# Performance work log

Hardware: AMD Instinct MI355X
Metric: run time of the kernel (lower is better)

The kernel has to match this reference:

```python
import jax, jax.numpy as jnp
import numpy as np

D_MODEL = 2048
N_HEADS = 16
D_HEAD = D_MODEL // N_HEADS
D_FF = 8192
EPS = 1e-5


def _xavier(key, shape):
    fan_out, fan_in = shape
    limit = np.sqrt(6.0 / (fan_in + fan_out))
    return jax.random.uniform(key, shape, jnp.float32, -limit, limit)


def setup_inputs() -> dict:
    key = jax.random.key(0)
    ks = jax.random.split(key, 6)
    B, S = 2, 2048
    x = jax.random.normal(ks[0], (B, S, D_MODEL), jnp.float32)
    # additive causal mask: 0 on/below diagonal, -inf above
    causal = jnp.tril(jnp.ones((S, S), jnp.bool_))
    mask = jnp.where(causal, 0.0, -1e9).astype(jnp.float32)
    return {
        "x": x,
        "mask": mask,
        "Wqkv": _xavier(ks[1], (3 * D_MODEL, D_MODEL)),
        "Wo": _xavier(ks[2], (D_MODEL, D_MODEL)),
        "w1": _xavier(ks[3], (D_FF, D_MODEL)),
        "w2": _xavier(ks[4], (D_MODEL, D_FF)),
        "ln1_g": jnp.ones((D_MODEL,), jnp.float32),
        "ln1_b": jnp.zeros((D_MODEL,), jnp.float32),
        "ln2_g": jnp.ones((D_MODEL,), jnp.float32),
        "ln2_b": jnp.zeros((D_MODEL,), jnp.float32),
    }


def _layernorm(x, g, b):
    mu = jnp.mean(x, axis=-1, keepdims=True)
    var = jnp.mean(jnp.square(x - mu), axis=-1, keepdims=True)
    return (x - mu) * jax.lax.rsqrt(var + EPS) * g + b


def reference(x, mask, Wqkv, Wo, w1, w2, ln1_g, ln1_b, ln2_g, ln2_b):
    B, S, D = x.shape
    # --- attention sublayer (pre-norm) ---
    h = _layernorm(x, ln1_g, ln1_b)
    qkv = (h @ Wqkv.T).reshape(B, S, 3, N_HEADS, D_HEAD)
    q, k, v = qkv[:, :, 0], qkv[:, :, 1], qkv[:, :, 2]  # [B,S,H,Dh]
    scores = jnp.einsum("bqhd,bkhd->bhqk", q, k) / np.sqrt(D_HEAD)
    scores = scores + mask  # broadcast [S,S] over [B,H,S,S]
    attn = jax.nn.softmax(scores, axis=-1)
    out = jnp.einsum("bhqk,bkhd->bqhd", attn, v).reshape(B, S, D)
    x = x + out @ Wo.T
    # --- FFN sublayer (pre-norm) ---
    h = _layernorm(x, ln2_g, ln2_b)
    x = x + jax.nn.gelu(h @ w1.T, approximate=False) @ w2.T
    return x
```

## Files before the change

kernel.cpp:

```cpp
#include <hip/hip_runtime.h>
#include <hip/hip_bf16.h>
#include <cmath>

#define D_MODEL 2048
#define N_HEADS 16
#define D_HEAD 128
#define D_FF 8192
#define S_LEN 2048
#define BATCH 2

typedef short bf16x8 __attribute__((ext_vector_type(8)));
typedef float f32x4 __attribute__((ext_vector_type(4)));
typedef unsigned short ushort_t;

__device__ __forceinline__ ushort_t f2bf(float f) {
  __hip_bfloat16 b = __float2bfloat16(f);
  union { __hip_bfloat16 b; ushort_t u; } cvt;
  cvt.b = b;
  return cvt.u;
}

__device__ __forceinline__ void gload16(const void* g, void* l) {
  __builtin_amdgcn_global_load_lds(
      (const __attribute__((address_space(1))) unsigned int*)g,
      (__attribute__((address_space(3))) unsigned int*)l, 16, 0, 0);
}

__device__ __forceinline__ float gelu_f(float v) {
  return 0.5f * v * (1.0f + erff(v * 0.70710678118654752f));
}

__global__ __launch_bounds__(256) void ln_bf16_kernel(
    const float* __restrict__ x, const float* __restrict__ g,
    const float* __restrict__ bb, ushort_t* __restrict__ outB) {
  const int row = blockIdx.x;
  const int tid = threadIdx.x;
  const float4* xr = (const float4*)(x + (size_t)row * D_MODEL);
  float4 v0 = xr[tid];
  float4 v1 = xr[tid + 256];
  float s  = v0.x + v0.y + v0.z + v0.w + v1.x + v1.y + v1.z + v1.w;
  float ss = v0.x*v0.x + v0.y*v0.y + v0.z*v0.z + v0.w*v0.w
           + v1.x*v1.x + v1.y*v1.y + v1.z*v1.z + v1.w*v1.w;
#pragma unroll
  for (int off = 32; off > 0; off >>= 1) {
    s  += __shfl_down(s, off);
    ss += __shfl_down(ss, off);
  }
  __shared__ float red[8];
  const int wid = tid >> 6;
  if ((tid & 63) == 0) { red[wid] = s; red[4 + wid] = ss; }
  __syncthreads();
  s  = red[0] + red[1] + red[2] + red[3];
  ss = red[4] + red[5] + red[6] + red[7];
  const float mu   = s * (1.0f / D_MODEL);
  const float var  = ss * (1.0f / D_MODEL) - mu * mu;
  const float rstd = rsqrtf(var + 1e-5f);
  const float4* gr = (const float4*)g;
  const float4* br = (const float4*)bb;
  float4 g0 = gr[tid], g1 = gr[tid + 256];
  float4 b0 = br[tid], b1 = br[tid + 256];
  ushort4 h0, h1;
  h0.x = f2bf((v0.x - mu) * rstd * g0.x + b0.x);
  h0.y = f2bf((v0.y - mu) * rstd * g0.y + b0.y);
  h0.z = f2bf((v0.z - mu) * rstd * g0.z + b0.z);
  h0.w = f2bf((v0.w - mu) * rstd * g0.w + b0.w);
  h1.x = f2bf((v1.x - mu) * rstd * g1.x + b1.x);
  h1.y = f2bf((v1.y - mu) * rstd * g1.y + b1.y);
  h1.z = f2bf((v1.z - mu) * rstd * g1.z + b1.z);
  h1.w = f2bf((v1.w - mu) * rstd * g1.w + b1.w);
  ushort4* oh = (ushort4*)(outB + (size_t)row * D_MODEL);
  oh[tid] = h0; oh[tid + 256] = h1;
}

__global__ __launch_bounds__(256) void wconv_kernel(
    const float* __restrict__ W, ushort_t* __restrict__ H, int n4) {
  for (int i = blockIdx.x * 256 + threadIdx.x; i < n4; i += gridDim.x * 256) {
    float4 v = ((const float4*)W)[i];
    ushort4 h;
    h.x = f2bf(v.x); h.y = f2bf(v.y); h.z = f2bf(v.z); h.w = f2bf(v.w);
    ((ushort4*)H)[i] = h;
  }
}

__global__ __launch_bounds__(256) void wconv_chunk_kernel(
    const float* __restrict__ W, ushort_t* __restrict__ H, int rows,
    int chunkCols, int rowStride, int colOff) {
  const int c4n = chunkCols >> 2;
  const int n4 = rows * c4n;
  for (int i = blockIdx.x * 256 + threadIdx.x; i < n4; i += gridDim.x * 256) {
    const int r = i / c4n, c4 = i - r * c4n;
    float4 v = *(const float4*)&W[(size_t)r * rowStride + colOff + c4 * 4];
    ushort4 h;
    h.x = f2bf(v.x); h.y = f2bf(v.y); h.z = f2bf(v.z); h.w = f2bf(v.w);
    ((ushort4*)H)[i] = h;
  }
}

template <int EPI>
__global__ __launch_bounds__(256, 4) void gemmb(
    const ushort_t* __restrict__ A, const ushort_t* __restrict__ B,
    const float* __restrict__ R, float* __restrict__ C,
    ushort_t* __restrict__ Cb, ushort_t* __restrict__ Q3,
    ushort_t* __restrict__ K3, ushort_t* __restrict__ V3,
    int M, int N, int K) {
  __shared__ char lds[2][16384];

  const int gX = gridDim.x;
  const int nwg = gX * gridDim.y;
  const int bid0 = blockIdx.y * gX + blockIdx.x;
  const int cpx = nwg >> 3;
  const int bid = (bid0 & 7) * cpx + (bid0 >> 3);
  const int bn0 = (bid % gX) * 128;
  const int bm0 = (bid / gX) * 128;

  const int tid = threadIdx.x;
  const int lane = tid & 63;
  const int wv = tid >> 6;
  const int wr = wv >> 1, wc = wv & 1;

  const int scs = (((lane & 7) ^ (lane >> 3)) << 4);
  const ushort_t* src = (wv < 2) ? A : B;
  const int rb0 = (wv < 2) ? bm0 : bn0;
  char* myLds = &lds[wv >> 1][0] + (wv & 1) * 8192;
  const ushort_t* srcBase =
      src + (size_t)(rb0 + (wv & 1) * 64 + (lane >> 3)) * K + (scs >> 1);

  const int l15 = lane & 15;
  const int swz = (lane & 7) << 4;
  const int cb0 = (((lane >> 4) * 16)) ^ swz;
  const int cb1 = (64 + ((lane >> 4) * 16)) ^ swz;

  f32x4 acc[4][4];
#pragma unroll
  for (int i = 0; i < 4; ++i)
#pragma unroll
    for (int j = 0; j < 4; ++j) acc[i][j] = (f32x4)0.0f;

  const char* ldsA = &lds[0][0];
  const char* ldsB = &lds[1][0];

  for (int kt = 0; kt < K; kt += 64) {
    {
      const ushort_t* g = srcBase + kt;
#pragma unroll
      for (int ch = 0; ch < 8; ++ch)
        gload16(g + (size_t)ch * 8 * K, myLds + ch * 1024);
    }
    __syncthreads();
#pragma unroll
    for (int ks = 0; ks < 2; ++ks) {
      const int cb = ks ? cb1 : cb0;
      bf16x8 af[4], bf[4];
#pragma unroll
      for (int mf = 0; mf < 4; ++mf)
        af[mf] = *(const bf16x8*)(ldsA + (wr * 64 + mf * 16 + l15) * 128 + cb);
#pragma unroll
      for (int nf = 0; nf < 4; ++nf)
        bf[nf] = *(const bf16x8*)(ldsB + (wc * 64 + nf * 16 + l15) * 128 + cb);
#pragma unroll
      for (int mf = 0; mf < 4; ++mf)
#pragma unroll
        for (int nf = 0; nf < 4; ++nf)
          acc[mf][nf] = __builtin_amdgcn_mfma_f32_16x16x32_bf16(
              af[mf], bf[nf], acc[mf][nf], 0, 0, 0);
    }
    __syncthreads();
  }

  const int orow = bm0 + wr * 64 + (lane >> 4) * 4;
  const int ocol = bn0 + wc * 64 + l15;
#pragma unroll
  for (int mf = 0; mf < 4; ++mf)
#pragma unroll
    for (int nf = 0; nf < 4; ++nf) {
      const f32x4 v = acc[mf][nf];
#pragma unroll
      for (int reg = 0; reg < 4; ++reg) {
        const int gr = orow + mf * 16 + reg;
        const int gcol = ocol + nf * 16;
        float f = v[reg];
        if (EPI == 1) {
          const size_t idx = (size_t)gr * N + gcol;
          C[idx] = f + R[idx];
        } else if (EPI == 2) {
          Cb[(size_t)gr * N + gcol] = f2bf(gelu_f(f));
        } else if (EPI == 3) {
          const ushort_t vb = f2bf(f);
          if (gcol < D_MODEL) {
            Q3[(size_t)gr * D_MODEL + gcol] = vb;
          } else {
            const int cc = gcol - D_MODEL;
            const bool isK = cc < D_MODEL;
            const int cc2 = isK ? cc : cc - D_MODEL;
            const int hh = cc2 >> 7, dd = cc2 & 127;
            const int bb = gr >> 11, ss = gr & 2047;
            const int tt = ss >> 6, rr = ss & 63;
            const size_t tb =
                ((size_t)((bb * N_HEADS + hh) * 32 + tt)) * 16384;
            if (isK) {
              const int byt = (rr * 256 + dd * 2) ^ ((rr & 7) << 4);
              *(ushort_t*)((char*)K3 + tb + byt) = vb;
            } else {
              const int byt = (dd * 128 + rr * 2) ^ ((dd & 7) << 4);
              *(ushort_t*)((char*)V3 + tb + byt) = vb;
            }
          }
        }
      }
    }
}

__global__ __launch_bounds__(256, 2) void attn_mfma_kernel(
    const ushort_t* __restrict__ Qc, const ushort_t* __restrict__ Kp,
    const ushort_t* __restrict__ Vp, ushort_t* __restrict__ outB) {
  const int pa = blockIdx.x, h = blockIdx.y, b = blockIdx.z;
  __shared__ char ldsK[16384];
  __shared__ char ldsVt[16384];
  __shared__ char ldsP[4][2048];
  const int tid = threadIdx.x, lane = tid & 63, w = tid >> 6;
  const int l15 = lane & 15, hi = lane >> 4;
  const int swzA = (l15 & 7) << 4;
  const float scale = 0.08838834764831845f;
  const size_t tbase0 = ((size_t)(b * N_HEADS + h) * 32) * 16384;

  for (int ph = 0; ph < 2; ++ph) {
    const int qc = ph ? (31 - pa) : pa;
    bf16x8 qf[4];
    {
      const int qrow = qc * 64 + w * 16 + l15;
      const ushort_t* qp =
          Qc + (size_t)(b * S_LEN + qrow) * D_MODEL + h * D_HEAD + hi * 8;
#pragma unroll
      for (int dt = 0; dt < 4; ++dt) qf[dt] = *(const bf16x8*)(qp + dt * 32);
    }
    float mrow[4], lrow[4];
#pragma unroll
    for (int r = 0; r < 4; ++r) { mrow[r] = -INFINITY; lrow[r] = 0.0f; }
    f32x4 oa[8];
#pragma unroll
    for (int dt = 0; dt < 8; ++dt) oa[dt] = (f32x4)0.0f;

    const int nkv = qc + 1;
    const int wqmax = qc * 64 + w * 16 + 15;

    for (int t = 0; t < nkv; ++t) {
      const int kv0 = t * 64;
      {
        const char* ks = (const char*)Kp + tbase0 + (size_t)t * 16384;
        const char* vs = (const char*)Vp + tbase0 + (size_t)t * 16384;
#pragma unroll
        for (int c = 0; c < 4; ++c) {
          gload16(ks + c * 4096 + tid * 16, ldsK + c * 4096 + tid * 16);
          gload16(vs + c * 4096 + tid * 16, ldsVt + c * 4096 + tid * 16);
        }
      }
      __syncthreads();
      if (kv0 <= wqmax) {
        f32x4 sa[4];
#pragma unroll
        for (int nt = 0; nt < 4; ++nt) sa[nt] = (f32x4)0.0f;
#pragma unroll
        for (int nt = 0; nt < 4; ++nt) {
          const int ro = (nt * 16 + l15) * 256;
#pragma unroll
          for (int dt = 0; dt < 4; ++dt) {
            bf16x8 kf =
                *(const bf16x8*)(ldsK + ro + ((dt * 64 + hi * 16) ^ swzA));
            sa[nt] = __builtin_amdgcn_mfma_f32_16x16x32_bf16(qf[dt], kf,
                                                             sa[nt], 0, 0, 0);
          }
        }
#pragma unroll
        for (int nt = 0; nt < 4; ++nt) {
          const int kg = kv0 + nt * 16 + l15;
#pragma unroll
          for (int r = 0; r < 4; ++r) {
            const int qg = qc * 64 + w * 16 + hi * 4 + r;
            float s = sa[nt][r] * scale;
            if (kg > qg) s -= 1e9f;
            sa[nt][r] = s;
          }
        }
        float frow[4];
#pragma unroll
        for (int r = 0; r < 4; ++r) {
          float tm = fmaxf(fmaxf(sa[0][r], sa[1][r]),
                           fmaxf(sa[2][r], sa[3][r]));
          tm = fmaxf(tm, __shfl_xor(tm, 1));
          tm = fmaxf(tm, __shfl_xor(tm, 2));
          tm = fmaxf(tm, __shfl_xor(tm, 4));
          tm = fmaxf(tm, __shfl_xor(tm, 8));
          const float mo = mrow[r];
          const float mn = fmaxf(mo, tm);
          const float fc = __expf(mo - mn);
          float sum = 0.0f;
#pragma unroll
          for (int nt = 0; nt < 4; ++nt) {
            const float p = __expf(sa[nt][r] - mn);
            sa[nt][r] = p;
            sum += p;
          }
          sum += __shfl_xor(sum, 1);
          sum += __shfl_xor(sum, 2);
          sum += __shfl_xor(sum, 4);
          sum += __shfl_xor(sum, 8);
          lrow[r] = lrow[r] * fc + sum;
          mrow[r] = mn;
          frow[r] = fc;
        }
        char* pw = ldsP[w];
#pragma unroll
        for (int r = 0; r < 4; ++r) {
          const int q = hi * 4 + r;
          const int qs = (q & 7) << 4;
#pragma unroll
          for (int nt = 0; nt < 4; ++nt) {
            const int byt = (q * 128 + (nt * 16 + l15) * 2) ^ qs;
            *(ushort_t*)(pw + byt) = f2bf(sa[nt][r]);
          }
        }
#pragma unroll
        for (int dt = 0; dt < 8; ++dt)
#pragma unroll
          for (int r = 0; r < 4; ++r) oa[dt][r] *= frow[r];
        bf16x8 pf[2];
#pragma unroll
        for (int kt = 0; kt < 2; ++kt)
          pf[kt] = *(const bf16x8*)(pw + (l15 * 128 +
                                          ((kt * 64 + hi * 16) ^ swzA)));
#pragma unroll
        for (int dt = 0; dt < 8; ++dt) {
          const int ro = (dt * 16 + l15) * 128;
#pragma unroll
          for (int kt = 0; kt < 2; ++kt) {
            bf16x8 vf =
                *(const bf16x8*)(ldsVt + ro + ((kt * 64 + hi * 16) ^ swzA));
            oa[dt] = __builtin_amdgcn_mfma_f32_16x16x32_bf16(pf[kt], vf,
                                                             oa[dt], 0, 0, 0);
          }
        }
      }
      __syncthreads();
    }
#pragma unroll
    for (int r = 0; r < 4; ++r) {
      const float linv = 1.0f / lrow[r];
      const size_t row = (size_t)(b * S_LEN + qc * 64 + w * 16 + hi * 4 + r);
#pragma unroll
      for (int dt = 0; dt < 8; ++dt) {
        const int col = h * D_HEAD + dt * 16 + l15;
        outB[row * D_MODEL + col] = f2bf(oa[dt][r] * linv);
      }
    }
  }
}

extern "C" void kernel_launch(void* const* d_in, const int* in_sizes, int n_in,
                              void* d_out, int out_size, void* d_ws,
                              size_t ws_size, hipStream_t stream) {
  const float* x    = (const float*)d_in[0];
  const float* Wqkv = (const float*)d_in[2];
  const float* Wo   = (const float*)d_in[3];
  const float* w1   = (const float*)d_in[4];
  const float* w2   = (const float*)d_in[5];
  const float* ln1g = (const float*)d_in[6];
  const float* ln1b = (const float*)d_in[7];
  const float* ln2g = (const float*)d_in[8];
  const float* ln2b = (const float*)d_in[9];
  float* out = (float*)d_out;

  const int M = BATCH * S_LEN;

  const size_t NEED = 92274688;
  if (ws_size < NEED) return;

  char* base = (char*)d_ws;
  ushort_t* WB  = (ushort_t*)base;
  ushort_t* act = (ushort_t*)(base + 25165824);
  ushort_t* Qc  = (ushort_t*)(base + 41943040);
  ushort_t* Kp  = (ushort_t*)(base + 58720256);
  ushort_t* Vp  = (ushort_t*)(base + 75497472);
  ushort_t* ffB = (ushort_t*)(base + 41943040);

  ln_bf16_kernel<<<M, 256, 0, stream>>>(x, ln1g, ln1b, act);
  wconv_kernel<<<2048, 256, 0, stream>>>(Wqkv, WB, 12582912 / 4);
  gemmb<3><<<dim3(3 * D_MODEL / 128, M / 128), 256, 0, stream>>>(
      act, WB, nullptr, nullptr, nullptr, Qc, Kp, Vp, M, 3 * D_MODEL, D_MODEL);
  attn_mfma_kernel<<<dim3(16, N_HEADS, BATCH), 256, 0, stream>>>(
      Qc, Kp, Vp, act);
  wconv_kernel<<<2048, 256, 0, stream>>>(Wo, WB, 4194304 / 4);
  gemmb<1><<<dim3(D_MODEL / 128, M / 128), 256, 0, stream>>>(
      act, WB, x, out, nullptr, nullptr, nullptr, nullptr,
      M, D_MODEL, D_MODEL);
  ln_bf16_kernel<<<M, 256, 0, stream>>>(out, ln2g, ln2b, act);
  for (int c = 0; c < 2; ++c) {
    wconv_kernel<<<2048, 256, 0, stream>>>(
        w1 + (size_t)c * 4096 * D_MODEL, WB, 8388608 / 4);
    gemmb<2><<<dim3(4096 / 128, M / 128), 256, 0, stream>>>(
        act, WB, nullptr, nullptr, ffB, nullptr, nullptr, nullptr,
        M, 4096, D_MODEL);
    wconv_chunk_kernel<<<2048, 256, 0, stream>>>(
        w2, WB, D_MODEL, 4096, D_FF, c * 4096);
    gemmb<1><<<dim3(D_MODEL / 128, M / 128), 256, 0, stream>>>(
        ffB, WB, out, out, nullptr, nullptr, nullptr, nullptr,
        M, D_MODEL, 4096);
  }
}
```

Measured before the change: 824.4 us.

## Replace GEMM with 8-wave 256-row tiled double-buffered pipelined kernel

Replaces the 128x128, 4-wave, single-buffered bf16 GEMM with a 512-thread kernel using 256xBN tiles (BN 256 or 128) and double-buffered LDS. Global-to-LDS loads for the next K tile are split into four stages interleaved with MFMA phases, using explicit vmcnt waits and raised wave priority. The aim is to hide global load latency and raise arithmetic intensity per block. In exchange it uses more LDS and registers per block, lowers occupancy, and produces fewer blocks for the smaller GEMMs.

```diff
diff --git a/kernel.cpp b/kernel.cpp
--- a/kernel.cpp
+++ b/kernel.cpp
@@ -28,6 +28,19 @@
 
 __device__ __forceinline__ float gelu_f(float v) {
   return 0.5f * v * (1.0f + erff(v * 0.70710678118654752f));
+}
+
+__device__ __forceinline__ void wait_vm4() {
+  asm volatile("s_waitcnt vmcnt(4)" ::: "memory");
+  __builtin_amdgcn_sched_barrier(0);
+}
+__device__ __forceinline__ void wait_vm3() {
+  asm volatile("s_waitcnt vmcnt(3)" ::: "memory");
+  __builtin_amdgcn_sched_barrier(0);
+}
+__device__ __forceinline__ void wait_vm0() {
+  asm volatile("s_waitcnt vmcnt(0)" ::: "memory");
+  __builtin_amdgcn_sched_barrier(0);
 }
 
 __global__ __launch_bounds__(256) void ln_bf16_kernel(
@@ -96,83 +109,150 @@
   }
 }
 
-template <int EPI>
-__global__ __launch_bounds__(256, 4) void gemmb(
+template <int EPI, int BN>
+__global__ __launch_bounds__(512, 2) void gemm8(
     const ushort_t* __restrict__ A, const ushort_t* __restrict__ B,
     const float* __restrict__ R, float* __restrict__ C,
     ushort_t* __restrict__ Cb, ushort_t* __restrict__ Q3,
     ushort_t* __restrict__ K3, ushort_t* __restrict__ V3,
     int M, int N, int K) {
-  __shared__ char lds[2][16384];
+  constexpr int APLANE = 16384;
+  constexpr int BPLANE = BN * 64;
+  constexpr int BUFSZ = 2 * APLANE + 2 * BPLANE;
+  constexpr int NF = BN / 64;
+  constexpr int WN = BN / 4;
+  __shared__ char lds[2 * BUFSZ];
 
   const int gX = gridDim.x;
   const int nwg = gX * gridDim.y;
   const int bid0 = blockIdx.y * gX + blockIdx.x;
   const int cpx = nwg >> 3;
   const int bid = (bid0 & 7) * cpx + (bid0 >> 3);
-  const int bn0 = (bid % gX) * 128;
-  const int bm0 = (bid / gX) * 128;
+  const int bn0 = (bid % gX) * BN;
+  const int bm0 = (bid / gX) * 256;
 
   const int tid = threadIdx.x;
   const int lane = tid & 63;
-  const int wv = tid >> 6;
-  const int wr = wv >> 1, wc = wv & 1;
-
-  const int scs = (((lane & 7) ^ (lane >> 3)) << 4);
-  const ushort_t* src = (wv < 2) ? A : B;
-  const int rb0 = (wv < 2) ? bm0 : bn0;
-  char* myLds = &lds[wv >> 1][0] + (wv & 1) * 8192;
-  const ushort_t* srcBase =
-      src + (size_t)(rb0 + (wv & 1) * 64 + (lane >> 3)) * K + (scs >> 1);
-
-  const int l15 = lane & 15;
-  const int swz = (lane & 7) << 4;
-  const int cb0 = (((lane >> 4) * 16)) ^ swz;
-  const int cb1 = (64 + ((lane >> 4) * 16)) ^ swz;
-
-  f32x4 acc[4][4];
-#pragma unroll
-  for (int i = 0; i < 4; ++i)
-#pragma unroll
-    for (int j = 0; j < 4; ++j) acc[i][j] = (f32x4)0.0f;
-
-  const char* ldsA = &lds[0][0];
-  const char* ldsB = &lds[1][0];
-
-  for (int kt = 0; kt < K; kt += 64) {
-    {
-      const ushort_t* g = srcBase + kt;
-#pragma unroll
-      for (int ch = 0; ch < 8; ++ch)
-        gload16(g + (size_t)ch * 8 * K, myLds + ch * 1024);
-    }
-    __syncthreads();
-#pragma unroll
-    for (int ks = 0; ks < 2; ++ks) {
-      const int cb = ks ? cb1 : cb0;
-      bf16x8 af[4], bf[4];
-#pragma unroll
-      for (int mf = 0; mf < 4; ++mf)
-        af[mf] = *(const bf16x8*)(ldsA + (wr * 64 + mf * 16 + l15) * 128 + cb);
-#pragma unroll
-      for (int nf = 0; nf < 4; ++nf)
-        bf[nf] = *(const bf16x8*)(ldsB + (wc * 64 + nf * 16 + l15) * 128 + cb);
-#pragma unroll
-      for (int mf = 0; mf < 4; ++mf)
-#pragma unroll
-        for (int nf = 0; nf < 4; ++nf)
-          acc[mf][nf] = __builtin_amdgcn_mfma_f32_16x16x32_bf16(
-              af[mf], bf[nf], acc[mf][nf], 0, 0, 0);
-    }
-    __syncthreads();
-  }
-
-  const int orow = bm0 + wr * 64 + (lane >> 4) * 4;
-  const int ocol = bn0 + wc * 64 + l15;
-#pragma unroll
-  for (int mf = 0; mf < 4; ++mf)
-#pragma unroll
-    for (int nf = 0; nf < 4; ++nf) {
+  const int wid = tid >> 6;
+  const int wm = wid >> 2, wn = wid & 3;
+  const int l15 = lane & 15, hi = lane >> 4;
+
+  const ushort_t* aSrc = A + (size_t)(bm0 + (tid >> 2)) * K + (tid & 3) * 8;
+  const ushort_t* bSrc = B + (size_t)(bn0 + (tid >> 2)) * K + (tid & 3) * 8;
+  const int ldsW = wid * 1024;
+
+  const int aFrag = (wm * 128 + l15) * 64 + hi * 16;
+  const int bFrag = (wn * WN + l15) * 64 + hi * 16;
+
+  f32x4 acc[8][NF];
+#pragma unroll
+  for (int i = 0; i < 8; ++i)
+#pragma unroll
+    for (int j = 0; j < NF; ++j) acc[i][j] = (f32x4)0.0f;
+
+  const int NT = K >> 6;
+
+  auto STAGE = [&](int u, int j) {
+    char* buf = lds + (u & 1) * BUFSZ;
+    const int kt = u * 64;
+    if (j & 1) {
+      const int ks = (j == 3);
+      char* d = buf + ks * APLANE + ldsW;
+      const ushort_t* s = aSrc + kt + ks * 32;
+      gload16(s, d);
+      gload16(s + (size_t)128 * K, d + 8192);
+    } else {
+      const int ks = (j == 2);
+      char* d = buf + 2 * APLANE + ks * BPLANE + ldsW;
+      const ushort_t* s = bSrc + kt + ks * 32;
+      gload16(s, d);
+      if (BN == 256) gload16(s + (size_t)128 * K, d + 8192);
+    }
+  };
+  auto WAIT_STEADY = [&]() { if (BN == 256) wait_vm4(); else wait_vm3(); };
+
+  STAGE(0, 0); STAGE(0, 1); STAGE(0, 2); STAGE(0, 3);
+  WAIT_STEADY();
+  __builtin_amdgcn_s_barrier();
+
+  for (int t = 0; t < NT; ++t) {
+    const bool pf = (t + 1 < NT);
+    const char* buf = lds + (t & 1) * BUFSZ;
+    bf16x8 af[4], bfr[NF];
+
+    if (pf) STAGE(t + 1, 0);
+#pragma unroll
+    for (int nf = 0; nf < NF; ++nf)
+      bfr[nf] = *(const bf16x8*)(buf + 2 * APLANE + bFrag + nf * 1024);
+#pragma unroll
+    for (int mf = 0; mf < 4; ++mf)
+      af[mf] = *(const bf16x8*)(buf + aFrag + mf * 1024);
+    __builtin_amdgcn_s_setprio(1);
+#pragma unroll
+    for (int mf = 0; mf < 4; ++mf)
+#pragma unroll
+      for (int nf = 0; nf < NF; ++nf)
+        acc[mf][nf] = __builtin_amdgcn_mfma_f32_16x16x32_bf16(
+            af[mf], bfr[nf], acc[mf][nf], 0, 0, 0);
+    __builtin_amdgcn_s_setprio(0);
+    __builtin_amdgcn_s_barrier();
+
+    if (pf) STAGE(t + 1, 1);
+#pragma unroll
+    for (int mf = 0; mf < 4; ++mf)
+      af[mf] = *(const bf16x8*)(buf + aFrag + (mf + 4) * 1024);
+    __builtin_amdgcn_s_setprio(1);
+#pragma unroll
+    for (int mf = 0; mf < 4; ++mf)
+#pragma unroll
+      for (int nf = 0; nf < NF; ++nf)
+        acc[mf + 4][nf] = __builtin_amdgcn_mfma_f32_16x16x32_bf16(
+            af[mf], bfr[nf], acc[mf + 4][nf], 0, 0, 0);
+    __builtin_amdgcn_s_setprio(0);
+    if (pf) WAIT_STEADY(); else wait_vm0();
+    __builtin_amdgcn_s_barrier();
+
+    if (pf) STAGE(t + 1, 2);
+#pragma unroll
+    for (int nf = 0; nf < NF; ++nf)
+      bfr[nf] = *(const bf16x8*)(buf + 2 * APLANE + BPLANE + bFrag + nf * 1024);
+#pragma unroll
+    for (int mf = 0; mf < 4; ++mf)
+      af[mf] = *(const bf16x8*)(buf + APLANE + aFrag + mf * 1024);
+    __builtin_amdgcn_s_setprio(1);
+#pragma unroll
+    for (int mf = 0; mf < 4; ++mf)
+#pragma unroll
+      for (int nf = 0; nf < NF; ++nf)
+        acc[mf][nf] = __builtin_amdgcn_mfma_f32_16x16x32_bf16(
+            af[mf], bfr[nf], acc[mf][nf], 0, 0, 0);
+    __builtin_amdgcn_s_setprio(0);
+    __builtin_amdgcn_s_barrier();
+
+    if (pf) STAGE(t + 1, 3);
+#pragma unroll
+    for (int mf = 0; mf < 4; ++mf)
+      af[mf] = *(const bf16x8*)(buf + APLANE + aFrag + (mf + 4) * 1024);
+    __builtin_amdgcn_s_setprio(1);
+#pragma unroll
+    for (int mf = 0; mf < 4; ++mf)
+#pragma unroll
+      for (int nf = 0; nf < NF; ++nf)
+        acc[mf + 4][nf] = __builtin_amdgcn_mfma_f32_16x16x32_bf16(
+            af[mf], bfr[nf], acc[mf + 4][nf], 0, 0, 0);
+    __builtin_amdgcn_s_setprio(0);
+    if (pf) {
+      WAIT_STEADY();
+      __builtin_amdgcn_s_barrier();
+    }
+  }
+
+  const int orow = bm0 + wm * 128 + hi * 4;
+  const int ocol = bn0 + wn * WN + l15;
+#pragma unroll
+  for (int mf = 0; mf < 8; ++mf)
+#pragma unroll
+    for (int nf = 0; nf < NF; ++nf) {
       const f32x4 v = acc[mf][nf];
 #pragma unroll
       for (int reg = 0; reg < 4; ++reg) {
@@ -193,8 +273,8 @@
             const bool isK = cc < D_MODEL;
             const int cc2 = isK ? cc : cc - D_MODEL;
             const int hh = cc2 >> 7, dd = cc2 & 127;
-            const int bb = gr >> 11, ss = gr & 2047;
-            const int tt = ss >> 6, rr = ss & 63;
+            const int bb = gr >> 11, ssr = gr & 2047;
+            const int tt = ssr >> 6, rr = ssr & 63;
             const size_t tb =
                 ((size_t)((bb * N_HEADS + hh) * 32 + tt)) * 16384;
             if (isK) {
@@ -384,24 +464,24 @@
 
   ln_bf16_kernel<<<M, 256, 0, stream>>>(x, ln1g, ln1b, act);
   wconv_kernel<<<2048, 256, 0, stream>>>(Wqkv, WB, 12582912 / 4);
-  gemmb<3><<<dim3(3 * D_MODEL / 128, M / 128), 256, 0, stream>>>(
+  gemm8<3, 256><<<dim3(3 * D_MODEL / 256, M / 256), 512, 0, stream>>>(
       act, WB, nullptr, nullptr, nullptr, Qc, Kp, Vp, M, 3 * D_MODEL, D_MODEL);
   attn_mfma_kernel<<<dim3(16, N_HEADS, BATCH), 256, 0, stream>>>(
       Qc, Kp, Vp, act);
   wconv_kernel<<<2048, 256, 0, stream>>>(Wo, WB, 4194304 / 4);
-  gemmb<1><<<dim3(D_MODEL / 128, M / 128), 256, 0, stream>>>(
+  gemm8<1, 128><<<dim3(D_MODEL / 128, M / 256), 512, 0, stream>>>(
       act, WB, x, out, nullptr, nullptr, nullptr, nullptr,
       M, D_MODEL, D_MODEL);
   ln_bf16_kernel<<<M, 256, 0, stream>>>(out, ln2g, ln2b, act);
   for (int c = 0; c < 2; ++c) {
     wconv_kernel<<<2048, 256, 0, stream>>>(
         w1 + (size_t)c * 4096 * D_MODEL, WB, 8388608 / 4);
-    gemmb<2><<<dim3(4096 / 128, M / 128), 256, 0, stream>>>(
+    gemm8<2, 256><<<dim3(4096 / 256, M / 256), 512, 0, stream>>>(
         act, WB, nullptr, nullptr, ffB, nullptr, nullptr, nullptr,
         M, 4096, D_MODEL);
     wconv_chunk_kernel<<<2048, 256, 0, stream>>>(
         w2, WB, D_MODEL, 4096, D_FF, c * 4096);
-    gemmb<1><<<dim3(D_MODEL / 128, M / 128), 256, 0, stream>>>(
+    gemm8<1, 128><<<dim3(D_MODEL / 128, M / 256), 512, 0, stream>>>(
         ffB, WB, out, out, nullptr, nullptr, nullptr, nullptr,
         M, D_MODEL, 4096);
   }
```

Measured after the change: 880.9 us. 1.07x slower.
